# Performance work log

Measured on AMD Instinct MI355X. Metric: run time of the kernel, lower is better.

## Reference

```python
import jax, jax.numpy as jnp
import numpy as np

SIGMA = 0.2
BN_EPS = 1e-5


def setup_inputs() -> dict:
    key = jax.random.key(0)
    k1, k2, k3, k4 = jax.random.split(key, 4)
    B, N, K = 8, 16384, 64
    normals = jax.random.normal(k1, (B, 3, N), dtype=jnp.float32)
    # normalize to unit normals (faithful to what the module consumes in practice)
    normals = normals / jnp.linalg.norm(normals, axis=1, keepdims=True)
    neighbor_idx = jax.random.randint(k2, (B, N, 3), 0, N, dtype=jnp.int64)
    weight_alpha = jax.random.uniform(k3, (1, K, 4), dtype=jnp.float32) * np.pi
    weight_beta = jax.random.uniform(k4, (1, K, 4), dtype=jnp.float32) * (2 * np.pi)
    bn_gamma = jnp.ones((K,), dtype=jnp.float32)
    bn_beta = jnp.zeros((K,), dtype=jnp.float32)
    return {
        "normals": normals,
        "neighbor_idx": neighbor_idx,
        "weight_alpha": weight_alpha,
        "weight_beta": weight_beta,
        "bn_gamma": bn_gamma,
        "bn_beta": bn_beta,
    }


def reference(normals, neighbor_idx, weight_alpha, weight_beta, bn_gamma, bn_beta):
    # normals: (B, 3, N); neighbor_idx: (B, N, 3)
    # kernel directions on unit sphere: W[c, k, m], c in xyz, m in 4 points per kernel
    W = jnp.concatenate(
        [
            jnp.sin(weight_alpha) * jnp.cos(weight_beta),
            jnp.sin(weight_alpha) * jnp.sin(weight_beta),
            jnp.cos(weight_alpha),
        ],
        axis=0,
    )  # (3, K, 4)

    # gather neighbor normals: nbr[b, c, i, j] = normals[b, c, neighbor_idx[b, i, j]]
    nbr = jax.vmap(lambda nm, idx: nm[:, idx])(normals, neighbor_idx)  # (B, 3, N, 3)
    F = jnp.concatenate([normals[:, :, :, None], nbr], axis=3)  # (B, 3, N, 4) face points p

    # squared distances via ||f||^2 + ||w||^2 - 2 f.w  (avoids 6D broadcast of torch code)
    dots = jnp.einsum("bcnp,ckm->bknpm", F, W)  # (B, K, N, 4, 4)
    F2 = jnp.sum(F * F, axis=1)[:, None, :, :, None]  # (B, 1, N, 4, 1)
    W2 = jnp.sum(W * W, axis=0)[None, :, None, None, :]  # (1, K, 1, 1, 4)
    dist = F2 + W2 - 2.0 * dots  # (B, K, N, 4, 4)

    inv = -1.0 / (2.0 * SIGMA * SIGMA)
    feat = jnp.sum(jnp.exp(dist * inv), axis=(3, 4)) / 16.0  # (B, K, N)

    # BatchNorm1d (training mode, biased variance over batch+spatial dims) + ReLU
    mean = jnp.mean(feat, axis=(0, 2), keepdims=True)
    var = jnp.var(feat, axis=(0, 2), keepdims=True)
    xhat = (feat - mean) * jax.lax.rsqrt(var + BN_EPS)
    out = bn_gamma[None, :, None] * xhat + bn_beta[None, :, None]
    return jax.nn.relu(out)
```

## Files before the change

kernel.cpp:

```cpp
#include <hip/hip_runtime.h>

#define BB 8
#define NN 16384
#define KK 64

__constant__ const float F_INV = -12.5f;
__constant__ const float F_M2INV = 25.0f;

__global__ __launch_bounds__(256) void fkc_main(
    const float* __restrict__ normals,
    const int*   __restrict__ nidx,
    const float* __restrict__ walpha,
    const float* __restrict__ wbeta,
    float* __restrict__ out,
    float* __restrict__ gsum,
    float* __restrict__ gss)
{
    __shared__ float Wx[KK * 4], Wy[KK * 4], Wz[KK * 4];
    __shared__ float psum[KK][4];
    __shared__ float pss[KK][4];

    const int tid = threadIdx.x;

    {
        float a = walpha[tid];
        float b = wbeta[tid];
        float sa = __sinf(a);
        Wx[tid] = sa * __cosf(b);
        Wy[tid] = sa * __sinf(b);
        Wz[tid] = __cosf(a);
    }
    __syncthreads();

    const int gid = blockIdx.x * 256 + tid;
    const int b = gid >> 14;
    const int n = gid & (NN - 1);
    const float* nb = normals + b * 3 * NN;

    float fx[4], fy[4], fz[4], e[4];
    fx[0] = nb[n];
    fy[0] = nb[NN + n];
    fz[0] = nb[2 * NN + n];
    const int ibase = (b * NN + n) * 3;
#pragma unroll
    for (int j = 0; j < 3; ++j) {
        int id = nidx[ibase + j];
        fx[j + 1] = nb[id];
        fy[j + 1] = nb[NN + id];
        fz[j + 1] = nb[2 * NN + id];
    }
#pragma unroll
    for (int p = 0; p < 4; ++p) {
        float n2 = fmaf(fx[p], fx[p], fmaf(fy[p], fy[p], fz[p] * fz[p]));
        e[p] = F_INV * (n2 + 1.0f);
    }

    const int lane = tid & 63;
    const int wv = tid >> 6;

    for (int k = 0; k < KK; ++k) {
        float acc = 0.0f;
#pragma unroll
        for (int m = 0; m < 4; ++m) {
            float wx = Wx[k * 4 + m];
            float wy = Wy[k * 4 + m];
            float wz = Wz[k * 4 + m];
#pragma unroll
            for (int p = 0; p < 4; ++p) {
                float d = fmaf(fx[p], wx, fmaf(fy[p], wy, fz[p] * wz));
                acc += __expf(fmaf(F_M2INV, d, e[p]));
            }
        }
        float feat = acc * (1.0f / 16.0f);
        out[(b * KK + k) * NN + n] = feat;

        float s = feat;
        float ss = feat * feat;
#pragma unroll
        for (int off = 1; off < 64; off <<= 1) {
            s  += __shfl_xor(s,  off, 64);
            ss += __shfl_xor(ss, off, 64);
        }
        if (lane == 0) { psum[k][wv] = s; pss[k][wv] = ss; }
    }
    __syncthreads();

    if (tid < KK) {
        float s  = psum[tid][0] + psum[tid][1] + psum[tid][2] + psum[tid][3];
        float ss = pss[tid][0] + pss[tid][1] + pss[tid][2] + pss[tid][3];
        atomicAdd(&gsum[tid], s);
        atomicAdd(&gss[tid], ss);
    }
}

__global__ __launch_bounds__(64) void fkc_stats(
    const float* __restrict__ gsum,
    const float* __restrict__ gss,
    const float* __restrict__ gamma,
    const float* __restrict__ beta,
    float* __restrict__ scale,
    float* __restrict__ shift)
{
    const int k = threadIdx.x;
    const float invM = 1.0f / (float)(BB * NN);
    float mean = gsum[k] * invM;
    float var = fmaf(-mean, mean, gss[k] * invM);
    float sc = gamma[k] * rsqrtf(var + 1e-5f);
    scale[k] = sc;
    shift[k] = fmaf(-mean, sc, beta[k]);
}

__global__ __launch_bounds__(256) void fkc_apply(
    float4* __restrict__ out4,
    const float* __restrict__ scale,
    const float* __restrict__ shift)
{
    const int i = blockIdx.x * 256 + threadIdx.x;
    const int k = (i >> 12) & (KK - 1);
    const float sc = scale[k];
    const float sh = shift[k];
    float4 v = out4[i];
    v.x = fmaxf(fmaf(v.x, sc, sh), 0.0f);
    v.y = fmaxf(fmaf(v.y, sc, sh), 0.0f);
    v.z = fmaxf(fmaf(v.z, sc, sh), 0.0f);
    v.w = fmaxf(fmaf(v.w, sc, sh), 0.0f);
    out4[i] = v;
}

extern "C" void kernel_launch(void* const* d_in, const int* in_sizes, int n_in,
                              void* d_out, int out_size, void* d_ws, size_t ws_size,
                              hipStream_t stream) {
    const float* normals = (const float*)d_in[0];
    const int*   nidx    = (const int*)d_in[1];
    const float* walpha  = (const float*)d_in[2];
    const float* wbeta   = (const float*)d_in[3];
    const float* gamma   = (const float*)d_in[4];
    const float* beta    = (const float*)d_in[5];
    float* out = (float*)d_out;
    float* ws = (float*)d_ws;

    float* gsum  = ws;
    float* gss   = ws + 64;
    float* scale = ws + 128;
    float* shift = ws + 192;

    hipMemsetAsync(ws, 0, 128 * sizeof(float), stream);

    const int total = BB * NN;
    fkc_main<<<total / 256, 256, 0, stream>>>(normals, nidx, walpha, wbeta,
                                              out, gsum, gss);
    fkc_stats<<<1, 64, 0, stream>>>(gsum, gss, gamma, beta, scale, shift);

    const int n4 = (BB * KK * NN) / 4;
    fkc_apply<<<n4 / 256, 256, 0, stream>>>((float4*)out, scale, shift);
}
```

Baseline: 134.1 us.

## Move BN statistics to a separate reduce pass and split K across blocks

The main kernel no longer does per-channel wave shuffle reductions and global atomics. It only computes features, and each block now handles half of the 64 channels, which doubles the block count. The exponent constants are folded into the weights so each term costs three FMAs plus a native exp2. A new reduce kernel re-reads the output to produce per-slice partial sums, and the apply kernel combines those partials itself, so the stats kernel and the memset are gone. The trade is one extra full read of the output buffer in exchange for removing the shuffle and atomic work from the compute-bound kernel. Features are also stored without the 1/16 scale, which changes how large BN epsilon is relative to the variance.

```diff
diff --git a/kernel.cpp b/kernel.cpp
--- a/kernel.cpp
+++ b/kernel.cpp
@@ -4,21 +4,24 @@
 #define NN 16384
 #define KK 64
 
-__constant__ const float F_INV = -12.5f;
-__constant__ const float F_M2INV = 25.0f;
+#if __has_builtin(__builtin_amdgcn_exp2f)
+#define EXP2(x) __builtin_amdgcn_exp2f(x)
+#else
+#define EXP2(x) exp2f(x)
+#endif
+
+#define LOG2E 1.44269504088896340736f
+#define CW (25.0f * LOG2E)
+#define CE (-12.5f * LOG2E)
 
 __global__ __launch_bounds__(256) void fkc_main(
     const float* __restrict__ normals,
     const int*   __restrict__ nidx,
     const float* __restrict__ walpha,
     const float* __restrict__ wbeta,
-    float* __restrict__ out,
-    float* __restrict__ gsum,
-    float* __restrict__ gss)
+    float* __restrict__ out)
 {
-    __shared__ float Wx[KK * 4], Wy[KK * 4], Wz[KK * 4];
-    __shared__ float psum[KK][4];
-    __shared__ float pss[KK][4];
+    __shared__ float4 WV[KK * 4];
 
     const int tid = threadIdx.x;
 
@@ -26,18 +29,20 @@
         float a = walpha[tid];
         float b = wbeta[tid];
         float sa = __sinf(a);
-        Wx[tid] = sa * __cosf(b);
-        Wy[tid] = sa * __sinf(b);
-        Wz[tid] = __cosf(a);
+        WV[tid] = make_float4(CW * sa * __cosf(b),
+                              CW * sa * __sinf(b),
+                              CW * __cosf(a), 0.0f);
     }
     __syncthreads();
 
-    const int gid = blockIdx.x * 256 + tid;
+    const int pg = blockIdx.x >> 1;
+    const int k0 = (blockIdx.x & 1) * 32;
+    const int gid = pg * 256 + tid;
     const int b = gid >> 14;
     const int n = gid & (NN - 1);
     const float* nb = normals + b * 3 * NN;
 
-    float fx[4], fy[4], fz[4], e[4];
+    float fx[4], fy[4], fz[4], e2[4];
     fx[0] = nb[n];
     fy[0] = nb[NN + n];
     fz[0] = nb[2 * NN + n];
@@ -52,73 +57,89 @@
 #pragma unroll
     for (int p = 0; p < 4; ++p) {
         float n2 = fmaf(fx[p], fx[p], fmaf(fy[p], fy[p], fz[p] * fz[p]));
-        e[p] = F_INV * (n2 + 1.0f);
+        e2[p] = CE * (n2 + 1.0f);
     }
 
-    const int lane = tid & 63;
-    const int wv = tid >> 6;
-
-    for (int k = 0; k < KK; ++k) {
+    float* orow = out + (b * KK + k0) * NN + n;
+#pragma unroll 2
+    for (int k = 0; k < 32; ++k) {
         float acc = 0.0f;
 #pragma unroll
         for (int m = 0; m < 4; ++m) {
-            float wx = Wx[k * 4 + m];
-            float wy = Wy[k * 4 + m];
-            float wz = Wz[k * 4 + m];
+            float4 w = WV[((k0 + k) << 2) + m];
 #pragma unroll
             for (int p = 0; p < 4; ++p) {
-                float d = fmaf(fx[p], wx, fmaf(fy[p], wy, fz[p] * wz));
-                acc += __expf(fmaf(F_M2INV, d, e[p]));
+                float arg = fmaf(fz[p], w.z,
+                            fmaf(fy[p], w.y,
+                            fmaf(fx[p], w.x, e2[p])));
+                acc += EXP2(arg);
             }
         }
-        float feat = acc * (1.0f / 16.0f);
-        out[(b * KK + k) * NN + n] = feat;
-
-        float s = feat;
-        float ss = feat * feat;
-#pragma unroll
-        for (int off = 1; off < 64; off <<= 1) {
-            s  += __shfl_xor(s,  off, 64);
-            ss += __shfl_xor(ss, off, 64);
-        }
-        if (lane == 0) { psum[k][wv] = s; pss[k][wv] = ss; }
-    }
-    __syncthreads();
-
-    if (tid < KK) {
-        float s  = psum[tid][0] + psum[tid][1] + psum[tid][2] + psum[tid][3];
-        float ss = pss[tid][0] + pss[tid][1] + pss[tid][2] + pss[tid][3];
-        atomicAdd(&gsum[tid], s);
-        atomicAdd(&gss[tid], ss);
+        orow[k * NN] = acc;
     }
 }
 
-__global__ __launch_bounds__(64) void fkc_stats(
-    const float* __restrict__ gsum,
-    const float* __restrict__ gss,
-    const float* __restrict__ gamma,
-    const float* __restrict__ beta,
-    float* __restrict__ scale,
-    float* __restrict__ shift)
+__global__ __launch_bounds__(256) void fkc_reduce(
+    const float4* __restrict__ out4,
+    float* __restrict__ psum,
+    float* __restrict__ pss)
 {
-    const int k = threadIdx.x;
-    const float invM = 1.0f / (float)(BB * NN);
-    float mean = gsum[k] * invM;
-    float var = fmaf(-mean, mean, gss[k] * invM);
-    float sc = gamma[k] * rsqrtf(var + 1e-5f);
-    scale[k] = sc;
-    shift[k] = fmaf(-mean, sc, beta[k]);
+    __shared__ float sw[4], ssw[4];
+    const int tid = threadIdx.x;
+    const int k = blockIdx.x >> 4;
+    const int c = blockIdx.x & 15;
+    const int b = c >> 1;
+    const int half = c & 1;
+    const int base4 = (b * KK + k) * (NN / 4) + half * 2048;
+
+    float s = 0.0f, ss = 0.0f;
+#pragma unroll
+    for (int i = 0; i < 8; ++i) {
+        float4 v = out4[base4 + tid + i * 256];
+        s += v.x + v.y + v.z + v.w;
+        ss += fmaf(v.x, v.x, fmaf(v.y, v.y, fmaf(v.z, v.z, v.w * v.w)));
+    }
+#pragma unroll
+    for (int off = 1; off < 64; off <<= 1) {
+        s  += __shfl_xor(s,  off, 64);
+        ss += __shfl_xor(ss, off, 64);
+    }
+    const int wv = tid >> 6;
+    if ((tid & 63) == 0) { sw[wv] = s; ssw[wv] = ss; }
+    __syncthreads();
+    if (tid == 0) {
+        psum[blockIdx.x] = sw[0] + sw[1] + sw[2] + sw[3];
+        pss[blockIdx.x]  = ssw[0] + ssw[1] + ssw[2] + ssw[3];
+    }
 }
 
 __global__ __launch_bounds__(256) void fkc_apply(
     float4* __restrict__ out4,
-    const float* __restrict__ scale,
-    const float* __restrict__ shift)
+    const float* __restrict__ psum,
+    const float* __restrict__ pss,
+    const float* __restrict__ gamma,
+    const float* __restrict__ beta)
 {
-    const int i = blockIdx.x * 256 + threadIdx.x;
+    __shared__ float s_tot, ss_tot;
+    const int tid = threadIdx.x;
+    const int i = blockIdx.x * 256 + tid;
     const int k = (i >> 12) & (KK - 1);
-    const float sc = scale[k];
-    const float sh = shift[k];
+
+    if (tid < 32) {
+        float v = (tid < 16) ? psum[k * 16 + tid] : pss[k * 16 + (tid - 16)];
+#pragma unroll
+        for (int off = 1; off < 16; off <<= 1) v += __shfl_xor(v, off, 64);
+        if (tid == 0)  s_tot = v;
+        if (tid == 16) ss_tot = v;
+    }
+    __syncthreads();
+
+    const float invM = 1.0f / (float)(BB * NN);
+    float mean = s_tot * invM;
+    float var = fmaf(-mean, mean, ss_tot * invM);
+    float sc = gamma[k] * rsqrtf(var + 1e-5f);
+    float sh = fmaf(-mean, sc, beta[k]);
+
     float4 v = out4[i];
     v.x = fmaxf(fmaf(v.x, sc, sh), 0.0f);
     v.y = fmaxf(fmaf(v.y, sc, sh), 0.0f);
@@ -139,18 +160,10 @@
     float* out = (float*)d_out;
     float* ws = (float*)d_ws;
 
-    float* gsum  = ws;
-    float* gss   = ws + 64;
-    float* scale = ws + 128;
-    float* shift = ws + 192;
+    float* psum = ws;
+    float* pss  = ws + 1024;
 
-    hipMemsetAsync(ws, 0, 128 * sizeof(float), stream);
-
-    const int total = BB * NN;
-    fkc_main<<<total / 256, 256, 0, stream>>>(normals, nidx, walpha, wbeta,
-                                              out, gsum, gss);
-    fkc_stats<<<1, 64, 0, stream>>>(gsum, gss, gamma, beta, scale, shift);
-
-    const int n4 = (BB * KK * NN) / 4;
-    fkc_apply<<<n4 / 256, 256, 0, stream>>>((float4*)out, scale, shift);
+    fkc_main<<<1024, 256, 0, stream>>>(normals, nidx, walpha, wbeta, out);
+    fkc_reduce<<<1024, 256, 0, stream>>>((const float4*)out, psum, pss);
+    fkc_apply<<<8192, 256, 0, stream>>>((float4*)out, psum, pss, gamma, beta);
 }
```

Measured after the change: 118.8 us. 11.4% less time.
